# Performance work log

Hardware: AMD Instinct MI355X
Metric: run time of the kernel (lower is better)

The kernel has to match this reference:

```python
import jax, jax.numpy as jnp
import numpy as np

B, S, D_MODEL, N_HEADS, HEAD_DIM = 4, 2048, 1024, 16, 64
NEG = -1e9


def apply_rope_real(x, cos_f, sin_f):
    # x: [B, H, S, D]; cos_f/sin_f: [S, D//2] broadcast over B, H
    x_even = x[..., ::2]
    x_odd = x[..., 1::2]
    out_even = x_even * cos_f - x_odd * sin_f
    out_odd = x_even * sin_f + x_odd * cos_f
    return jnp.stack([out_even, out_odd], axis=-1).reshape(x.shape)


def setup_inputs() -> dict:
    key = jax.random.key(0)
    ks = jax.random.split(key, 8)
    x = jax.random.normal(ks[0], (B, S, D_MODEL), dtype=jnp.float32)
    # RoPE tables: theta_i = 10000^{-2i/d}, angles = pos * theta
    inv_freq = 1.0 / (10000.0 ** (jnp.arange(0, HEAD_DIM, 2, dtype=jnp.float32) / HEAD_DIM))
    angles = jnp.arange(S, dtype=jnp.float32)[:, None] * inv_freq[None, :]  # [S, D/2]
    cos_freqs = jnp.cos(angles)
    sin_freqs = jnp.sin(angles)
    causal_mask = jnp.where(jnp.tril(jnp.ones((S, S), dtype=bool)), 0.0, NEG).astype(jnp.float32)
    scale = 0.02
    w_q = jax.random.normal(ks[1], (D_MODEL, D_MODEL), dtype=jnp.float32) * scale
    w_k = jax.random.normal(ks[2], (D_MODEL, D_MODEL), dtype=jnp.float32) * scale
    w_v = jax.random.normal(ks[3], (D_MODEL, D_MODEL), dtype=jnp.float32) * scale
    w_o = jax.random.normal(ks[4], (D_MODEL, D_MODEL), dtype=jnp.float32) * scale
    return {"x": x, "cos_freqs": cos_freqs, "sin_freqs": sin_freqs,
            "causal_mask": causal_mask, "w_q": w_q, "w_k": w_k, "w_v": w_v, "w_o": w_o}


def reference(x, cos_freqs, sin_freqs, causal_mask, w_q, w_k, w_v, w_o):
    batch, seq_len, _ = x.shape
    scale = 1.0 / jnp.sqrt(jnp.float32(HEAD_DIM))
    # torch Linear: y = x @ W.T
    def proj(w):
        return (x @ w.T).reshape(batch, seq_len, N_HEADS, HEAD_DIM).transpose(0, 2, 1, 3)
    q = apply_rope_real(proj(w_q), cos_freqs, sin_freqs)
    k = apply_rope_real(proj(w_k), cos_freqs, sin_freqs)
    v = proj(w_v)
    attn = jnp.einsum('bhqd,bhkd->bhqk', q, k) * scale + causal_mask
    attn = jax.nn.softmax(attn, axis=-1)
    out = jnp.einsum('bhqk,bhkd->bhqd', attn, v)
    out = out.transpose(0, 2, 1, 3).reshape(batch, seq_len, -1)
    return out @ w_o.T
```

## Files before the change

### kernel.cpp

```cpp
#include <hip/hip_runtime.h>
#include <stdint.h>

#define B_  4
#define S_  2048
#define DM_ 1024
#define NH_ 16
#define HD_ 64

typedef unsigned short ushort_t;
typedef __bf16 bf16x8 __attribute__((ext_vector_type(8)));
typedef float  floatx4 __attribute__((ext_vector_type(4)));
typedef float  floatx16 __attribute__((ext_vector_type(16)));

__device__ __forceinline__ float bf2f(ushort_t u) {
    union { unsigned int i; float f; } v; v.i = ((unsigned int)u) << 16; return v.f;
}
__device__ __forceinline__ ushort_t f2bf(float f) {
    union { float f; unsigned int i; } v; v.f = f;
    unsigned int x = v.i;
    return (ushort_t)((x + 0x7fffu + ((x >> 16) & 1u)) >> 16);
}
__device__ __forceinline__ unsigned int pack_bf16_trunc(float lo, float hi) {
    union { float f; unsigned int u; } a, b;
    a.f = lo; b.f = hi;
    return __builtin_amdgcn_perm(b.u, a.u, 0x07060302u);
}

__global__ __launch_bounds__(256) void cvt_all_kernel(
    const float* __restrict__ x,  const float* __restrict__ wq,
    const float* __restrict__ wk, const float* __restrict__ wv,
    const float* __restrict__ wo,
    ushort_t* __restrict__ xb,  ushort_t* __restrict__ wqb,
    ushort_t* __restrict__ wkb, ushort_t* __restrict__ wvb,
    ushort_t* __restrict__ wob)
{
    const int blk = blockIdx.x;
    const float* src; ushort_t* dst; int off;
    if (blk < 8192)       { src = x;  dst = xb;  off = blk; }
    else if (blk < 9216)  { src = wq; dst = wqb; off = blk - 8192; }
    else if (blk < 10240) { src = wk; dst = wkb; off = blk - 9216; }
    else if (blk < 11264) { src = wv; dst = wvb; off = blk - 10240; }
    else                  { src = wo; dst = wob; off = blk - 11264; }
    const int i = off * 256 + threadIdx.x;
    float4 v = ((const float4*)src)[i];
    ushort4 o; o.x = f2bf(v.x); o.y = f2bf(v.y); o.z = f2bf(v.z); o.w = f2bf(v.w);
    ((ushort4*)dst)[i] = o;
}

__global__ __launch_bounds__(512, 2) void gemm_bt_kernel(
    const ushort_t* __restrict__ A,
    const ushort_t* __restrict__ B0, const ushort_t* __restrict__ B1,
    const ushort_t* __restrict__ B2,
    void* __restrict__ C0, void* __restrict__ C1, void* __restrict__ C2,
    int M, int N, int K, int mode, int nz)
{
    __shared__ ushort_t As[2][16384];
    __shared__ ushort_t Bs[2][8192];

    const int lid = blockIdx.x;
    const int cpx = gridDim.x >> 3;
    const int wg  = (lid & 7) * cpx + (lid >> 3);
    const int x   = wg / (8 * nz);
    const int rr  = wg - x * (8 * nz);
    const int y   = rr & 7;
    const int z   = rr >> 3;

    const ushort_t* Bw = z == 0 ? B0 : z == 1 ? B1 : B2;
    void* Cv           = z == 0 ? C0 : z == 1 ? C1 : C2;

    const int tid  = threadIdx.x;
    const int wave = tid >> 6, lane = tid & 63;
    const int l15 = lane & 15, quad = lane >> 4;
    const int wr = wave >> 1, wc = wave & 1;
    const int mbase = x * 256;
    const int nbase = y * 128;
    const int NT = K >> 6;

    auto stageA = [&](int bt, int t, int L0) {
#pragma unroll
        for (int L = L0; L < L0 + 2; ++L) {
            const int e8  = L * 512 + tid;
            const int row = e8 >> 3, c = e8 & 7;
            const ushort_t* src = A + (size_t)(mbase + row) * K + t * 64 + ((c ^ (row & 7)) << 3);
            __builtin_amdgcn_global_load_lds(
                (const __attribute__((address_space(1))) unsigned int*)src,
                (__attribute__((address_space(3))) unsigned int*)(&As[bt][e8 * 8]), 16, 0, 0);
        }
    };
    auto stageB = [&](int bt, int t, int L) {
        const int e8  = L * 512 + tid;
        const int row = e8 >> 3, c = e8 & 7;
        const ushort_t* src = Bw + (size_t)(nbase + row) * K + t * 64 + ((c ^ (row & 7)) << 3);
        __builtin_amdgcn_global_load_lds(
            (const __attribute__((address_space(1))) unsigned int*)src,
            (__attribute__((address_space(3))) unsigned int*)(&Bs[bt][e8 * 8]), 16, 0, 0);
    };

    floatx4 acc[4][4] = {};

    stageA(0, 0, 0); stageA(0, 0, 2);
    stageB(0, 0, 0); stageB(0, 0, 1);
    if (NT > 1) {
        stageB(1, 1, 0); stageB(1, 1, 1);
        asm volatile("s_waitcnt vmcnt(2)" ::: "memory");
    } else {
        asm volatile("s_waitcnt vmcnt(0)" ::: "memory");
    }
    __builtin_amdgcn_s_barrier();

    auto do_tile = [&](int t, int bt) {
        bf16x8 a0[2][2], a1[2][2], b0[2][2], b1[2][2];
#pragma unroll
        for (int kk = 0; kk < 2; ++kk) {
#pragma unroll
            for (int f = 0; f < 2; ++f) {
                const int row = wr * 64 + f * 16 + l15;
                a0[kk][f] = *(const bf16x8*)&As[bt][row * 64 + ((((kk << 2) | quad)) ^ (l15 & 7)) * 8];
            }
#pragma unroll
            for (int g = 0; g < 2; ++g) {
                const int row = wc * 64 + g * 16 + l15;
                b0[kk][g] = *(const bf16x8*)&Bs[bt][row * 64 + ((((kk << 2) | quad)) ^ (l15 & 7)) * 8];
            }
        }
        if (t + 1 < NT) stageA(bt ^ 1, t + 1, 0);
        __builtin_amdgcn_s_barrier();
        asm volatile("s_waitcnt lgkmcnt(0)" ::: "memory");
        __builtin_amdgcn_s_setprio(1);
#pragma unroll
        for (int kk = 0; kk < 2; ++kk)
#pragma unroll
            for (int mt = 0; mt < 2; ++mt)
#pragma unroll
                for (int nt = 0; nt < 2; ++nt)
                    acc[mt][nt] = __builtin_amdgcn_mfma_f32_16x16x32_bf16(
                        a0[kk][mt], b0[kk][nt], acc[mt][nt], 0, 0, 0);
        __builtin_amdgcn_s_setprio(0);
        __builtin_amdgcn_s_barrier();

#pragma unroll
        for (int kk = 0; kk < 2; ++kk)
#pragma unroll
            for (int g = 0; g < 2; ++g) {
                const int row = wc * 64 + 32 + g * 16 + l15;
                b1[kk][g] = *(const bf16x8*)&Bs[bt][row * 64 + ((((kk << 2) | quad)) ^ (l15 & 7)) * 8];
            }
        if (t + 1 < NT) stageA(bt ^ 1, t + 1, 2);
        __builtin_amdgcn_s_barrier();
        asm volatile("s_waitcnt lgkmcnt(0)" ::: "memory");
        __builtin_amdgcn_s_setprio(1);
#pragma unroll
        for (int kk = 0; kk < 2; ++kk)
#pragma unroll
            for (int mt = 0; mt < 2; ++mt)
#pragma unroll
                for (int nt = 0; nt < 2; ++nt)
                    acc[mt][2 + nt] = __builtin_amdgcn_mfma_f32_16x16x32_bf16(
                        a0[kk][mt], b1[kk][nt], acc[mt][2 + nt], 0, 0, 0);
        __builtin_amdgcn_s_setprio(0);
        __builtin_amdgcn_s_barrier();

#pragma unroll
        for (int kk = 0; kk < 2; ++kk)
#pragma unroll
            for (int f = 0; f < 2; ++f) {
                const int row = wr * 64 + 32 + f * 16 + l15;
                a1[kk][f] = *(const bf16x8*)&As[bt][row * 64 + ((((kk << 2) | quad)) ^ (l15 & 7)) * 8];
            }
        if (t + 2 < NT) stageB(bt, t + 2, 0);
        __builtin_amdgcn_s_barrier();
        asm volatile("s_waitcnt lgkmcnt(0)" ::: "memory");
        __builtin_amdgcn_s_setprio(1);
#pragma unroll
        for (int kk = 0; kk < 2; ++kk)
#pragma unroll
            for (int mt = 0; mt < 2; ++mt)
#pragma unroll
                for (int nt = 0; nt < 2; ++nt)
                    acc[2 + mt][2 + nt] = __builtin_amdgcn_mfma_f32_16x16x32_bf16(
                        a1[kk][mt], b1[kk][nt], acc[2 + mt][2 + nt], 0, 0, 0);
        __builtin_amdgcn_s_setprio(0);
        __builtin_amdgcn_s_barrier();

        if (t + 2 < NT) stageB(bt, t + 2, 1);
        __builtin_amdgcn_s_barrier();
        __builtin_amdgcn_s_setprio(1);
#pragma unroll
        for (int kk = 0; kk < 2; ++kk)
#pragma unroll
            for (int mt = 0; mt < 2; ++mt)
#pragma unroll
                for (int nt = 0; nt < 2; ++nt)
                    acc[2 + mt][nt] = __builtin_amdgcn_mfma_f32_16x16x32_bf16(
                        a1[kk][mt], b0[kk][nt], acc[2 + mt][nt], 0, 0, 0);
        __builtin_amdgcn_s_setprio(0);
        if (t + 2 < NT) { asm volatile("s_waitcnt vmcnt(2)" ::: "memory"); }
        else            { asm volatile("s_waitcnt vmcnt(0)" ::: "memory"); }
        __builtin_amdgcn_s_barrier();
    };

    for (int t = 0; t < NT; t += 2) {
        do_tile(t, 0);
        do_tile(t + 1, 1);
    }

    const bool vtmode = (mode == 0) && (z == 2);
#pragma unroll
    for (int mt = 0; mt < 4; ++mt) {
#pragma unroll
        for (int nt = 0; nt < 4; ++nt) {
            const int col = nbase + wc * 64 + nt * 16 + l15;
            const int m0  = mbase + wr * 64 + mt * 16 + quad * 4;
            if (vtmode) {
                const int b = m0 >> 11, s = m0 & 2047;
                const int hh = col >> 6, d = col & 63;
                uint2 pk;
                pk.x = (unsigned)f2bf(acc[mt][nt][0]) | ((unsigned)f2bf(acc[mt][nt][1]) << 16);
                pk.y = (unsigned)f2bf(acc[mt][nt][2]) | ((unsigned)f2bf(acc[mt][nt][3]) << 16);
                *(uint2*)&((ushort_t*)Cv)[((size_t)((b * NH_ + hh) * HD_ + d)) * S_ + s] = pk;
            } else if (mode == 0) {
#pragma unroll
                for (int r = 0; r < 4; ++r) {
                    const int m = m0 + r;
                    const int b = m >> 11, s = m & 2047;
                    const int hh = col >> 6, d = col & 63;
                    ((ushort_t*)Cv)[(((size_t)(b * NH_ + hh)) * S_ + s) * HD_ + d] =
                        f2bf(acc[mt][nt][r]);
                }
            } else {
#pragma unroll
                for (int r = 0; r < 4; ++r)
                    ((float*)Cv)[(size_t)(m0 + r) * N + col] = acc[mt][nt][r];
            }
        }
    }
}

#define QSCALE 0.1803368801f
__global__ __launch_bounds__(256) void rope_kernel(
    ushort_t* __restrict__ q, ushort_t* __restrict__ k,
    const float* __restrict__ cf, const float* __restrict__ sf)
{
    const int idx = blockIdx.x * 256 + threadIdx.x;
    const int j = idx & 31;
    const int s = (idx >> 5) & (S_ - 1);
    const float c  = cf[s * 32 + j];
    const float sn = sf[s * 32 + j];
    const size_t base = (size_t)idx * 2;
    float qe = bf2f(q[base]), qo = bf2f(q[base + 1]);
    q[base]     = f2bf((qe * c - qo * sn) * QSCALE);
    q[base + 1] = f2bf((qe * sn + qo * c) * QSCALE);
    float ke = bf2f(k[base]), ko = bf2f(k[base + 1]);
    k[base]     = f2bf(ke * c - ko * sn);
    k[base + 1] = f2bf(ke * sn + ko * c);
}

__global__ __launch_bounds__(256, 2) void attn_kernel(
    const ushort_t* __restrict__ Qg, const ushort_t* __restrict__ Kg,
    const ushort_t* __restrict__ Vg, ushort_t* __restrict__ Og)
{
    __shared__ ushort_t Ks[64 * 72];
    __shared__ ushort_t Vt[64 * 72];
    __shared__ ushort_t Pt[4][32 * 64];

    const int pair = blockIdx.x;
    const int bh   = blockIdx.y;
    const int tid  = threadIdx.x;
    const int wave = tid >> 6, lane = tid & 63;
    const int l31 = lane & 31, h = lane >> 5;

    const size_t bh_off = (size_t)bh * S_ * HD_;
    const int trow = tid >> 3;
    const int tcol = (tid & 7) * 8;
    const int pswz = (l31 & 7) << 3;
    const int b_out = bh >> 4, h_out = bh & 15;

#pragma unroll 1
    for (int seg = 0; seg < 2; ++seg) {
        const int qtile = seg ? (15 - pair) : pair;
        const int qbase = qtile * 128;
        const int nkt   = 2 * qtile + 2;
        const int qrow  = qbase + wave * 32 + l31;

        bf16x8 qf[4];
#pragma unroll
        for (int ks = 0; ks < 4; ++ks)
            qf[ks] = *(const bf16x8*)(Qg + bh_off + (size_t)qrow * HD_ + ks * 16 + h * 8);

        float m_run = -1e30f, l_run = 0.f;
        floatx16 o_acc[2] = {};

        for (int kt = 0; kt < nkt; ++kt) {
            const int kbase = kt * 64;
            __syncthreads();
#pragma unroll
            for (int r = 0; r < 2; ++r) {
                const int row = trow + r * 32;
                *(bf16x8*)(Ks + row * 72 + tcol) =
                    *(const bf16x8*)(Kg + bh_off + (size_t)(kbase + row) * HD_ + tcol);
                const int c = tid + r * 256;
                const int d = c >> 3, k0 = (c & 7) * 8;
                bf16x8 vv = *(const bf16x8*)(Vg + bh_off + (size_t)d * S_ + kbase + k0);
                *(bf16x8*)(Vt + d * 72 + (k0 ^ (((d >> 3) & 7) << 3))) = vv;
            }
            __syncthreads();

            if (kbase > qbase + wave * 32 + 31) continue;

            floatx16 st[2] = {};
#pragma unroll
            for (int nt = 0; nt < 2; ++nt) {
                const ushort_t* kr = Ks + (nt * 32 + l31) * 72 + h * 8;
#pragma unroll
                for (int ks = 0; ks < 4; ++ks) {
                    bf16x8 kf = *(const bf16x8*)(kr + ks * 16);
                    st[nt] = __builtin_amdgcn_mfma_f32_32x32x16_bf16(kf, qf[ks], st[nt], 0, 0, 0);
                }
            }
            if (kbase + 63 > qbase + wave * 32) {
#pragma unroll
                for (int nt = 0; nt < 2; ++nt) {
                    const int key0 = kbase + nt * 32 + 4 * h;
#pragma unroll
                    for (int c = 0; c < 4; ++c)
#pragma unroll
                        for (int r = 0; r < 4; ++r)
                            if (key0 + 8 * c + r > qrow) st[nt][c * 4 + r] = -1e9f;
                }
            }
            float mx = st[0][0];
#pragma unroll
            for (int nt = 0; nt < 2; ++nt)
#pragma unroll
                for (int i = 0; i < 16; ++i) mx = fmaxf(mx, st[nt][i]);
            mx = fmaxf(mx, __shfl_xor(mx, 32, 64));
            const float mnew = fmaxf(m_run, mx);
            const float alpha = __builtin_amdgcn_exp2f(m_run - mnew);
            m_run = mnew;
            float sum = 0.f;
#pragma unroll
            for (int nt = 0; nt < 2; ++nt)
#pragma unroll
                for (int i = 0; i < 16; ++i) {
                    const float p = __builtin_amdgcn_exp2f(st[nt][i] - mnew);
                    st[nt][i] = p; sum += p;
                }
            sum += __shfl_xor(sum, 32, 64);
            l_run = l_run * alpha + sum;
#pragma unroll
            for (int dt = 0; dt < 2; ++dt)
#pragma unroll
                for (int i = 0; i < 16; ++i) o_acc[dt][i] *= alpha;

            ushort_t* pr = &Pt[wave][l31 * 64];
#pragma unroll
            for (int nt = 0; nt < 2; ++nt)
#pragma unroll
                for (int c = 0; c < 4; ++c) {
                    uint2 pk;
                    pk.x = pack_bf16_trunc(st[nt][c * 4 + 0], st[nt][c * 4 + 1]);
                    pk.y = pack_bf16_trunc(st[nt][c * 4 + 2], st[nt][c * 4 + 3]);
                    *(uint2*)(pr + (((nt * 32 + 8 * c) ^ pswz) + 4 * h)) = pk;
                }
            __builtin_amdgcn_fence(__ATOMIC_ACQ_REL, "wavefront");
            __builtin_amdgcn_wave_barrier();

            bf16x8 pf[4];
#pragma unroll
            for (int ks = 0; ks < 4; ++ks)
                pf[ks] = *(const bf16x8*)(&Pt[wave][l31 * 64 + ((ks * 16 + h * 8) ^ pswz)]);

#pragma unroll
            for (int dt = 0; dt < 2; ++dt) {
                const int d = dt * 32 + l31;
                const int sw = ((d >> 3) & 7) << 3;
                const ushort_t* vr = Vt + d * 72;
#pragma unroll
                for (int ks = 0; ks < 4; ++ks) {
                    bf16x8 vf = *(const bf16x8*)(vr + ((ks * 16 + h * 8) ^ sw));
                    o_acc[dt] = __builtin_amdgcn_mfma_f32_32x32x16_bf16(vf, pf[ks], o_acc[dt], 0, 0, 0);
                }
            }
        }

        const float inv = 1.0f / l_run;
        ushort_t* orow = Og + ((size_t)(b_out * S_ + qrow)) * DM_ + h_out * HD_;
#pragma unroll
        for (int dt = 0; dt < 2; ++dt)
#pragma unroll
            for (int c = 0; c < 4; ++c) {
                uint2 pk;
                pk.x = (unsigned)f2bf(o_acc[dt][c * 4 + 0] * inv) |
                       ((unsigned)f2bf(o_acc[dt][c * 4 + 1] * inv) << 16);
                pk.y = (unsigned)f2bf(o_acc[dt][c * 4 + 2] * inv) |
                       ((unsigned)f2bf(o_acc[dt][c * 4 + 3] * inv) << 16);
                *(uint2*)(orow + dt * 32 + 8 * c + 4 * h) = pk;
            }
    }
}

extern "C" void kernel_launch(void* const* d_in, const int* in_sizes, int n_in,
                              void* d_out, int out_size, void* d_ws, size_t ws_size,
                              hipStream_t stream)
{
    const float* x  = (const float*)d_in[0];
    const float* cf = (const float*)d_in[1];
    const float* sf = (const float*)d_in[2];
    const float* wq = (const float*)d_in[4];
    const float* wk = (const float*)d_in[5];
    const float* wv = (const float*)d_in[6];
    const float* wo = (const float*)d_in[7];
    float* out = (float*)d_out;

    const size_t NELEM = (size_t)B_ * S_ * DM_;
    const size_t WELEM = (size_t)DM_ * DM_;
    ushort_t* xb  = (ushort_t*)d_ws;
    ushort_t* qb  = xb + NELEM;
    ushort_t* kb  = qb + NELEM;
    ushort_t* vb  = kb + NELEM;
    ushort_t* ao  = vb + NELEM;
    ushort_t* wqb = ao + NELEM;
    ushort_t* wkb = wqb + WELEM;
    ushort_t* wvb = wkb + WELEM;
    ushort_t* wob = wvb + WELEM;

    cvt_all_kernel<<<dim3(8192 + 4 * 1024), 256, 0, stream>>>(
        x, wq, wk, wv, wo, xb, wqb, wkb, wvb, wob);

    const int M = B_ * S_;
    gemm_bt_kernel<<<dim3(32 * 8 * 3), 512, 0, stream>>>(
        xb, wqb, wkb, wvb, qb, kb, vb, M, DM_, DM_, 0, 3);
    rope_kernel<<<dim3((B_ * NH_ * S_ * 32) / 256), 256, 0, stream>>>(qb, kb, cf, sf);
    attn_kernel<<<dim3(8, B_ * NH_), 256, 0, stream>>>(qb, kb, vb, ao);
    gemm_bt_kernel<<<dim3(32 * 8), 512, 0, stream>>>(
        ao, wob, wob, wob, out, out, out, M, DM_, DM_, 1, 1);
}
```

Baseline: 282.1 us.

## Double-buffer K/V tiles with direct global-to-LDS async loads in attention

The attention kernel now keeps two LDS buffers for K and V and issues global_load_lds for the next 64-key tile before computing on the current one, so the fetch overlaps with the MFMA and softmax work. Staging through registers goes away, and the LDS layout moves from padded rows to an XOR-swizzled 64-wide layout. One barrier per iteration replaces two. LDS use roughly doubles for K/V, which could reduce occupancy at two blocks per CU, and each iteration still waits with vmcnt(0) before its barrier.

Result: no change. 285.8 us (+1.3%).

```diff
diff --git a/kernel.cpp b/kernel.cpp
--- a/kernel.cpp
+++ b/kernel.cpp
@@ -259,8 +259,8 @@
     const ushort_t* __restrict__ Qg, const ushort_t* __restrict__ Kg,
     const ushort_t* __restrict__ Vg, ushort_t* __restrict__ Og)
 {
-    __shared__ ushort_t Ks[64 * 72];
-    __shared__ ushort_t Vt[64 * 72];
+    __shared__ ushort_t Ks[2][64 * 64];
+    __shared__ ushort_t Vt[2][64 * 64];
     __shared__ ushort_t Pt[4][32 * 64];
 
     const int pair = blockIdx.x;
@@ -270,10 +270,12 @@
     const int l31 = lane & 31, h = lane >> 5;
 
     const size_t bh_off = (size_t)bh * S_ * HD_;
-    const int trow = tid >> 3;
-    const int tcol = (tid & 7) * 8;
     const int pswz = (l31 & 7) << 3;
     const int b_out = bh >> 4, h_out = bh & 15;
+
+    const int e0 = tid, e1 = tid + 256;
+    const int r0 = e0 >> 3, c0 = (e0 & 7) ^ (r0 & 7);
+    const int r1 = e1 >> 3, c1 = (e1 & 7) ^ (r1 & 7);
 
 #pragma unroll 1
     for (int seg = 0; seg < 2; ++seg) {
@@ -290,97 +292,130 @@
         float m_run = -1e30f, l_run = 0.f;
         floatx16 o_acc[2] = {};
 
+        {
+            const ushort_t* ka = Kg + bh_off + (size_t)r0 * HD_ + c0 * 8;
+            const ushort_t* kb = Kg + bh_off + (size_t)r1 * HD_ + c1 * 8;
+            const ushort_t* va = Vg + bh_off + (size_t)r0 * S_ + c0 * 8;
+            const ushort_t* vb = Vg + bh_off + (size_t)r1 * S_ + c1 * 8;
+            __builtin_amdgcn_global_load_lds(
+                (const __attribute__((address_space(1))) unsigned int*)ka,
+                (__attribute__((address_space(3))) unsigned int*)(&Ks[0][e0 * 8]), 16, 0, 0);
+            __builtin_amdgcn_global_load_lds(
+                (const __attribute__((address_space(1))) unsigned int*)kb,
+                (__attribute__((address_space(3))) unsigned int*)(&Ks[0][e1 * 8]), 16, 0, 0);
+            __builtin_amdgcn_global_load_lds(
+                (const __attribute__((address_space(1))) unsigned int*)va,
+                (__attribute__((address_space(3))) unsigned int*)(&Vt[0][e0 * 8]), 16, 0, 0);
+            __builtin_amdgcn_global_load_lds(
+                (const __attribute__((address_space(1))) unsigned int*)vb,
+                (__attribute__((address_space(3))) unsigned int*)(&Vt[0][e1 * 8]), 16, 0, 0);
+        }
+        asm volatile("s_waitcnt vmcnt(0)" ::: "memory");
+        __syncthreads();
+
         for (int kt = 0; kt < nkt; ++kt) {
             const int kbase = kt * 64;
+            const int cur = kt & 1;
+
+            if (kt + 1 < nkt) {
+                const int nb = kbase + 64;
+                const ushort_t* ka = Kg + bh_off + (size_t)(nb + r0) * HD_ + c0 * 8;
+                const ushort_t* kb = Kg + bh_off + (size_t)(nb + r1) * HD_ + c1 * 8;
+                const ushort_t* va = Vg + bh_off + (size_t)r0 * S_ + nb + c0 * 8;
+                const ushort_t* vb = Vg + bh_off + (size_t)r1 * S_ + nb + c1 * 8;
+                __builtin_amdgcn_global_load_lds(
+                    (const __attribute__((address_space(1))) unsigned int*)ka,
+                    (__attribute__((address_space(3))) unsigned int*)(&Ks[cur ^ 1][e0 * 8]), 16, 0, 0);
+                __builtin_amdgcn_global_load_lds(
+                    (const __attribute__((address_space(1))) unsigned int*)kb,
+                    (__attribute__((address_space(3))) unsigned int*)(&Ks[cur ^ 1][e1 * 8]), 16, 0, 0);
+                __builtin_amdgcn_global_load_lds(
+                    (const __attribute__((address_space(1))) unsigned int*)va,
+                    (__attribute__((address_space(3))) unsigned int*)(&Vt[cur ^ 1][e0 * 8]), 16, 0, 0);
+                __builtin_amdgcn_global_load_lds(
+                    (const __attribute__((address_space(1))) unsigned int*)vb,
+                    (__attribute__((address_space(3))) unsigned int*)(&Vt[cur ^ 1][e1 * 8]), 16, 0, 0);
+            }
+
+            if (kbase <= qbase + wave * 32 + 31) {
+                floatx16 st[2] = {};
+#pragma unroll
+                for (int nt = 0; nt < 2; ++nt) {
+                    const int krow = nt * 32 + l31;
+#pragma unroll
+                    for (int ks = 0; ks < 4; ++ks) {
+                        bf16x8 kf = *(const bf16x8*)&Ks[cur][krow * 64 +
+                                        (((ks * 2 + h) ^ (l31 & 7)) << 3)];
+                        st[nt] = __builtin_amdgcn_mfma_f32_32x32x16_bf16(kf, qf[ks], st[nt], 0, 0, 0);
+                    }
+                }
+                if (kbase + 63 > qbase + wave * 32) {
+#pragma unroll
+                    for (int nt = 0; nt < 2; ++nt) {
+                        const int key0 = kbase + nt * 32 + 4 * h;
+#pragma unroll
+                        for (int c = 0; c < 4; ++c)
+#pragma unroll
+                            for (int r = 0; r < 4; ++r)
+                                if (key0 + 8 * c + r > qrow) st[nt][c * 4 + r] = -1e9f;
+                    }
+                }
+                float mx = st[0][0];
+#pragma unroll
+                for (int nt = 0; nt < 2; ++nt)
+#pragma unroll
+                    for (int i = 0; i < 16; ++i) mx = fmaxf(mx, st[nt][i]);
+                mx = fmaxf(mx, __shfl_xor(mx, 32, 64));
+                const float mnew = fmaxf(m_run, mx);
+                const float alpha = __builtin_amdgcn_exp2f(m_run - mnew);
+                m_run = mnew;
+                float sum = 0.f;
+#pragma unroll
+                for (int nt = 0; nt < 2; ++nt)
+#pragma unroll
+                    for (int i = 0; i < 16; ++i) {
+                        const float p = __builtin_amdgcn_exp2f(st[nt][i] - mnew);
+                        st[nt][i] = p; sum += p;
+                    }
+                sum += __shfl_xor(sum, 32, 64);
+                l_run = l_run * alpha + sum;
+#pragma unroll
+                for (int dt = 0; dt < 2; ++dt)
+#pragma unroll
+                    for (int i = 0; i < 16; ++i) o_acc[dt][i] *= alpha;
+
+                ushort_t* pr = &Pt[wave][l31 * 64];
+#pragma unroll
+                for (int nt = 0; nt < 2; ++nt)
+#pragma unroll
+                    for (int c = 0; c < 4; ++c) {
+                        uint2 pk;
+                        pk.x = pack_bf16_trunc(st[nt][c * 4 + 0], st[nt][c * 4 + 1]);
+                        pk.y = pack_bf16_trunc(st[nt][c * 4 + 2], st[nt][c * 4 + 3]);
+                        *(uint2*)(pr + (((nt * 32 + 8 * c) ^ pswz) + 4 * h)) = pk;
+                    }
+                __builtin_amdgcn_fence(__ATOMIC_ACQ_REL, "wavefront");
+                __builtin_amdgcn_wave_barrier();
+
+                bf16x8 pf[4];
+#pragma unroll
+                for (int ks = 0; ks < 4; ++ks)
+                    pf[ks] = *(const bf16x8*)(&Pt[wave][l31 * 64 + ((ks * 16 + h * 8) ^ pswz)]);
+
+#pragma unroll
+                for (int dt = 0; dt < 2; ++dt) {
+                    const int d = dt * 32 + l31;
+#pragma unroll
+                    for (int ks = 0; ks < 4; ++ks) {
+                        bf16x8 vf = *(const bf16x8*)&Vt[cur][d * 64 +
+                                        (((ks * 2 + h) ^ (l31 & 7)) << 3)];
+                        o_acc[dt] = __builtin_amdgcn_mfma_f32_32x32x16_bf16(vf, pf[ks], o_acc[dt], 0, 0, 0);
+                    }
+                }
+            }
+
+            asm volatile("s_waitcnt vmcnt(0)" ::: "memory");
             __syncthreads();
-#pragma unroll
-            for (int r = 0; r < 2; ++r) {
-                const int row = trow + r * 32;
-                *(bf16x8*)(Ks + row * 72 + tcol) =
-                    *(const bf16x8*)(Kg + bh_off + (size_t)(kbase + row) * HD_ + tcol);
-                const int c = tid + r * 256;
-                const int d = c >> 3, k0 = (c & 7) * 8;
-                bf16x8 vv = *(const bf16x8*)(Vg + bh_off + (size_t)d * S_ + kbase + k0);
-                *(bf16x8*)(Vt + d * 72 + (k0 ^ (((d >> 3) & 7) << 3))) = vv;
-            }
-            __syncthreads();
-
-            if (kbase > qbase + wave * 32 + 31) continue;
-
-            floatx16 st[2] = {};
-#pragma unroll
-            for (int nt = 0; nt < 2; ++nt) {
-                const ushort_t* kr = Ks + (nt * 32 + l31) * 72 + h * 8;
-#pragma unroll
-                for (int ks = 0; ks < 4; ++ks) {
-                    bf16x8 kf = *(const bf16x8*)(kr + ks * 16);
-                    st[nt] = __builtin_amdgcn_mfma_f32_32x32x16_bf16(kf, qf[ks], st[nt], 0, 0, 0);
-                }
-            }
-            if (kbase + 63 > qbase + wave * 32) {
-#pragma unroll
-                for (int nt = 0; nt < 2; ++nt) {
-                    const int key0 = kbase + nt * 32 + 4 * h;
-#pragma unroll
-                    for (int c = 0; c < 4; ++c)
-#pragma unroll
-                        for (int r = 0; r < 4; ++r)
-                            if (key0 + 8 * c + r > qrow) st[nt][c * 4 + r] = -1e9f;
-                }
-            }
-            float mx = st[0][0];
-#pragma unroll
-            for (int nt = 0; nt < 2; ++nt)
-#pragma unroll
-                for (int i = 0; i < 16; ++i) mx = fmaxf(mx, st[nt][i]);
-            mx = fmaxf(mx, __shfl_xor(mx, 32, 64));
-            const float mnew = fmaxf(m_run, mx);
-            const float alpha = __builtin_amdgcn_exp2f(m_run - mnew);
-            m_run = mnew;
-            float sum = 0.f;
-#pragma unroll
-            for (int nt = 0; nt < 2; ++nt)
-#pragma unroll
-                for (int i = 0; i < 16; ++i) {
-                    const float p = __builtin_amdgcn_exp2f(st[nt][i] - mnew);
-                    st[nt][i] = p; sum += p;
-                }
-            sum += __shfl_xor(sum, 32, 64);
-            l_run = l_run * alpha + sum;
-#pragma unroll
-            for (int dt = 0; dt < 2; ++dt)
-#pragma unroll
-                for (int i = 0; i < 16; ++i) o_acc[dt][i] *= alpha;
-
-            ushort_t* pr = &Pt[wave][l31 * 64];
-#pragma unroll
-            for (int nt = 0; nt < 2; ++nt)
-#pragma unroll
-                for (int c = 0; c < 4; ++c) {
-                    uint2 pk;
-                    pk.x = pack_bf16_trunc(st[nt][c * 4 + 0], st[nt][c * 4 + 1]);
-                    pk.y = pack_bf16_trunc(st[nt][c * 4 + 2], st[nt][c * 4 + 3]);
-                    *(uint2*)(pr + (((nt * 32 + 8 * c) ^ pswz) + 4 * h)) = pk;
-                }
-            __builtin_amdgcn_fence(__ATOMIC_ACQ_REL, "wavefront");
-            __builtin_amdgcn_wave_barrier();
-
-            bf16x8 pf[4];
-#pragma unroll
-            for (int ks = 0; ks < 4; ++ks)
-                pf[ks] = *(const bf16x8*)(&Pt[wave][l31 * 64 + ((ks * 16 + h * 8) ^ pswz)]);
-
-#pragma unroll
-            for (int dt = 0; dt < 2; ++dt) {
-                const int d = dt * 32 + l31;
-                const int sw = ((d >> 3) & 7) << 3;
-                const ushort_t* vr = Vt + d * 72;
-#pragma unroll
-                for (int ks = 0; ks < 4; ++ks) {
-                    bf16x8 vf = *(const bf16x8*)(vr + ((ks * 16 + h * 8) ^ sw));
-                    o_acc[dt] = __builtin_amdgcn_mfma_f32_32x32x16_bf16(vf, pf[ks], o_acc[dt], 0, 0, 0);
-                }
-            }
         }
 
         const float inv = 1.0f / l_run;
```
